# Performance work log

Measured on AMD Instinct MI355X. Metric: run time of the kernel, lower is better.

## Reference

```python
import jax, jax.numpy as jnp
import numpy as np

B, T, V, S, I, G = 2, 4096, 1024, 256, 2048, 128


def setup_inputs() -> dict:
    key = jax.random.key(0)
    ks = jax.random.split(key, 10)
    n = lambda k, shape, std: jax.random.normal(k, shape, dtype=jnp.float32) * std
    return {
        "x": jax.random.normal(ks[0], (B, T, V), dtype=jnp.float32),
        # shared CausalMemory projections (torch Linear weight layout [out,in])
        "Wq": n(ks[1], (S, V), 0.02),
        "Wk": n(ks[2], (S, V), 0.02),
        "Wv": n(ks[3], (S, V), 0.02),
        "Wo": n(ks[4], (V, S), 0.02),
        # Delta
        "delta_logits": jnp.full((V,), 4.0, dtype=jnp.float32),
        "delta_scale": jnp.float32(0.1),
        # Theta / Gamma decay params
        "theta_decay": jnp.float32(4.0),
        "theta_scale": jnp.float32(0.1),
        "gamma_decay": jnp.float32(1.0),
        "gamma_scale": jnp.float32(0.1),
        # Alpha gate
        "alpha_down": n(ks[5], (G, V), 0.02),
        "alpha_up": n(ks[6], (V, G), 0.01),
        "alpha_up_b": jnp.full((V,), 2.0, dtype=jnp.float32),
        # Beta MLP
        "beta_down": n(ks[7], (I, V), 0.02),
        "beta_up": n(ks[8], (V, I), 0.02),
        "beta_bias": jnp.zeros((I,), dtype=jnp.float32),
        "beta_scale": jnp.float32(0.1),
    }


def _rmsnorm(x):
    eps = jnp.finfo(x.dtype).eps
    return x * jax.lax.rsqrt(jnp.mean(x * x, axis=-1, keepdims=True) + eps)


def _delta(x, decay_logits, scale):
    # causal EMA via weighted cumsum, matching torch reference exactly
    t = x.shape[1]
    decay = jax.nn.sigmoid(decay_logits)
    log_decay = jnp.log(jnp.clip(decay, 1e-06))
    steps = jnp.arange(t, dtype=x.dtype)[::-1]            # [T]
    w = jnp.exp(steps[:, None] * log_decay[None, :])      # [T,V]
    cum = jnp.cumsum(x * w[None], axis=1)
    cum = jnp.concatenate([jnp.zeros_like(cum[:, :1]), cum[:, :-1]], axis=1)
    return cum / jnp.clip(w[None], 1e-08) * scale


def _memory(x, Wq, Wk, Wv, Wo, decay_logit, scale):
    t = x.shape[1]
    q = x @ Wq.T
    k = x @ Wk.T
    v = x @ Wv.T
    scores = jnp.einsum("btd,bsd->bts", q, k)             # [B,T,T]
    decay = jax.nn.sigmoid(decay_logit)
    pos = jnp.arange(t)
    diff = pos[None, :] - pos[:, None]                    # j - i
    w = decay ** jnp.clip(diff.astype(x.dtype) - 1.0, 0.0, None) * (diff > 0)
    retrieved = jnp.einsum("bts,bsd->btd", scores * w[None], v)
    return (retrieved @ Wo.T) * scale


def _alpha(x, down, up, up_b):
    gate = jax.nn.sigmoid((x @ down.T) @ up.T + up_b)
    return x * gate


def _beta(x, down, up, bias, scale):
    h = jax.nn.gelu(x @ down.T + bias, approximate=False)
    return (h @ up.T) * scale


def reference(x, Wq, Wk, Wv, Wo, delta_logits, delta_scale, theta_decay,
              theta_scale, gamma_decay, gamma_scale, alpha_down, alpha_up,
              alpha_up_b, beta_down, beta_up, beta_bias, beta_scale):
    x = x + _delta(_rmsnorm(x), delta_logits, delta_scale)
    x = x + _memory(_rmsnorm(x), Wq, Wk, Wv, Wo, theta_decay, theta_scale)
    x = _alpha(x, alpha_down, alpha_up, alpha_up_b)
    x = x + _beta(_rmsnorm(x), beta_down, beta_up, beta_bias, beta_scale)
    x = x + _memory(_rmsnorm(x), Wq, Wk, Wv, Wo, gamma_decay, gamma_scale)
    return x
```

## Files before the change

kernel.cpp:

```cpp
#include <hip/hip_runtime.h>

typedef __attribute__((ext_vector_type(8))) short s16x8;
typedef __attribute__((ext_vector_type(4))) float f32x4;
typedef unsigned short u16;

#define DEV __device__ __forceinline__

DEV u16 f2b(float f) {
  unsigned u = __builtin_bit_cast(unsigned, f);
  unsigned r = (u + 0x7FFFu + ((u >> 16) & 1u)) >> 16;
  return (u16)r;
}
DEV float b2f(u16 h) { return __builtin_bit_cast(float, (unsigned)h << 16); }
DEV f32x4 mfma16(s16x8 a, s16x8 b, f32x4 c) {
  return __builtin_amdgcn_mfma_f32_16x16x32_bf16(a, b, c, 0, 0, 0);
}
DEV float sigmoidf_(float x) { return 1.0f / (1.0f + expf(-x)); }

DEV void g2l16(const u16* g, u16* l) {
  __builtin_amdgcn_global_load_lds((const __attribute__((address_space(1))) void*)g,
                                   (__attribute__((address_space(3))) void*)l, 16, 0, 0);
}

#define BAR() __builtin_amdgcn_s_barrier()
#define WAITV8() asm volatile("s_waitcnt vmcnt(8)" ::: "memory")
#define WAITV4() asm volatile("s_waitcnt vmcnt(4)" ::: "memory")
#define WAITV0() asm volatile("s_waitcnt vmcnt(0)" ::: "memory")
#define WAITL0()                                         \
  do {                                                   \
    asm volatile("s_waitcnt lgkmcnt(0)" ::: "memory");   \
    __builtin_amdgcn_sched_barrier(0);                   \
  } while (0)

__global__ __launch_bounds__(256) void cast_all(
    const float* __restrict__ Wq, const float* __restrict__ Wk, const float* __restrict__ Wv,
    const float* __restrict__ Wo, const float* __restrict__ adw, const float* __restrict__ auw,
    const float* __restrict__ bdw, const float* __restrict__ buw,
    u16* __restrict__ Wqkvb, u16* __restrict__ Wob, u16* __restrict__ adb,
    u16* __restrict__ aub, u16* __restrict__ bdb, u16* __restrict__ bub) {
  const int b = blockIdx.x;
  const float* s;
  u16* d;
  int rb;
  if (b < 768) {
    s = (b < 256) ? Wq : (b < 512) ? Wk : Wv;
    rb = (b < 256) ? b : (b < 512) ? (b - 256) : (b - 512);
    d = Wqkvb + ((b < 256) ? 0 : (b < 512) ? 262144 : 524288);
  } else if (b < 1024) { s = Wo;  d = Wob; rb = b - 768; }
  else if (b < 1152)   { s = adw; d = adb; rb = b - 1024; }
  else if (b < 1280)   { s = auw; d = aub; rb = b - 1152; }
  else if (b < 3328)   { s = bdw; d = bdb; rb = b - 1280; }
  else                 { s = buw; d = bub; rb = b - 3328; }
  size_t i = ((size_t)rb * 256 + threadIdx.x) * 4;
  float4 v = *(const float4*)(s + i);
  ushort4 p; p.x = f2b(v.x); p.y = f2b(v.y); p.z = f2b(v.z); p.w = f2b(v.w);
  *(ushort4*)(d + i) = p;
}

__global__ __launch_bounds__(256) void rmsnorm_k(const float* __restrict__ x, u16* __restrict__ y) {
  const size_t row = blockIdx.x;
  const int tid = threadIdx.x;
  float4 v = ((const float4*)(x + row * 1024))[tid];
  float ss = v.x * v.x + v.y * v.y + v.z * v.z + v.w * v.w;
#pragma unroll
  for (int o = 32; o >= 1; o >>= 1) ss += __shfl_xor(ss, o);
  __shared__ float red[4];
  if ((tid & 63) == 0) red[tid >> 6] = ss;
  __syncthreads();
  float tot = red[0] + red[1] + red[2] + red[3];
  float rn = rsqrtf(tot * (1.0f / 1024.0f) + 1.1920929e-7f);
  ushort4 p;
  p.x = f2b(v.x * rn); p.y = f2b(v.y * rn); p.z = f2b(v.z * rn); p.w = f2b(v.w * rn);
  *(ushort4*)(y + row * 1024 + tid * 4) = p;
}

__global__ __launch_bounds__(256)
void delta_partial(const u16* __restrict__ y, const float* __restrict__ logits, float* __restrict__ Pp) {
  const int v = blockIdx.x * 256 + threadIdx.x;
  const int c = blockIdx.y, b = blockIdx.z;
  const float dec = sigmoidf_(logits[v]);
  const float ldc = logf(fmaxf(dec, 1e-6f));
  const float dc = expf(ldc);
  const u16* yp = y + ((size_t)b * 4096 + c * 128) * 1024 + v;
  float wv = expf((float)(4095 - (c * 128 + 127)) * ldc);
  float acc = 0.0f;
  for (int t = 127; t >= 0; --t) {
    acc += b2f(yp[(size_t)t * 1024]) * wv;
    wv *= dc;
  }
  Pp[((size_t)b * 32 + c) * 1024 + v] = acc;
}

__global__ __launch_bounds__(256) void delta_scan(float* __restrict__ Pp) {
  const int v = blockIdx.x * 256 + threadIdx.x;
  const int b = blockIdx.y;
  float run = 0.0f;
  for (int c = 0; c < 32; ++c) {
    size_t i = ((size_t)b * 32 + c) * 1024 + v;
    float t = Pp[i];
    Pp[i] = run;
    run += t;
  }
}

__global__ __launch_bounds__(256)
void delta_apply(const float* __restrict__ x0, const u16* __restrict__ y,
                 const float* __restrict__ logits, const float* __restrict__ scale_p,
                 const float* __restrict__ Pp, float* __restrict__ x1) {
  const int v = blockIdx.x * 256 + threadIdx.x;
  const int c = blockIdx.y, b = blockIdx.z;
  const float dec = sigmoidf_(logits[v]);
  const float ldc = logf(fmaxf(dec, 1e-6f));
  const float dc = expf(ldc);
  const float invd = expf(-ldc);
  const float sc = scale_p[0];
  float wv = expf((float)(4095 - c * 128) * ldc);
  float iw = expf(-(float)(4095 - c * 128) * ldc);
  float carry = Pp[((size_t)b * 32 + c) * 1024 + v];
  size_t base = ((size_t)b * 4096 + c * 128) * 1024 + v;
  for (int t = 0; t < 128; ++t) {
    size_t idx = base + (size_t)t * 1024;
    x1[idx] = x0[idx] + carry * fminf(iw, 1e8f) * sc;
    carry += b2f(y[idx]) * wv;
    wv *= invd;
    iw *= dc;
  }
}

template <int EPI>
__global__ __launch_bounds__(256, 2)
void pgemm(const u16* __restrict__ A, const u16* __restrict__ Bw,
           int M, int N, int K,
           u16* __restrict__ Cb,
           const float* __restrict__ Xin, float* __restrict__ Xout,
           u16* __restrict__ Xb16,
           const float* __restrict__ bias, const float* __restrict__ scale_p,
           u16* __restrict__ P1, u16* __restrict__ P2, u16* __restrict__ P3) {
  __shared__ u16 sm[32768];
  const int tid = threadIdx.x;
  const int wid = tid >> 6, lane = tid & 63;
  const int gx = gridDim.x;
  const int id = blockIdx.y * gx + blockIdx.x;
  const int q8 = (gx * gridDim.y) >> 3;
  const int nid = (id & 7) * q8 + (id >> 3);
  const int bx = nid % gx, by = nid / gx;
  const int n0 = bx * 128, m0 = by * 128;
  const int wm = (wid >> 1) * 64, wn = (wid & 1) * 64;
  const int lr = lane & 15, lkc = lane >> 4;
  const int sw = lr & 7;
  const int c0 = (lkc ^ sw) * 8, c1 = ((lkc + 4) ^ sw) * 8;
  const int NT = K >> 6;
  const int srow = lane >> 3;
  const int scol = ((lane & 7) ^ srow) * 8;
  const u16* Ag = A + (size_t)(m0 + wid * 8 + srow) * K + scol;
  const u16* Bg = Bw + (size_t)(n0 + wid * 8 + srow) * K + scol;
  u16* const AL0 = sm;          u16* const BL0 = sm + 8192;
  u16* const AL1 = sm + 16384;  u16* const BL1 = sm + 24576;

  f32x4 acc[4][4] = {};

  auto STA = [&](int tau) {
    const u16* g = Ag + (size_t)tau * 64;
    u16* l = ((tau & 1) ? AL1 : AL0) + wid * 512;
#pragma unroll
    for (int c = 0; c < 4; ++c) g2l16(g + (size_t)c * 32 * K, l + c * 2048);
  };
  auto STB = [&](int tau) {
    const u16* g = Bg + (size_t)tau * 64;
    u16* l = ((tau & 1) ? BL1 : BL0) + wid * 512;
#pragma unroll
    for (int c = 0; c < 4; ++c) g2l16(g + (size_t)c * 32 * K, l + c * 2048);
  };
  auto RDA = [&](int tau, s16x8 (&d)[4][2]) {
    const u16* Ab = (tau & 1) ? AL1 : AL0;
#pragma unroll
    for (int i = 0; i < 4; ++i) {
      int base = (wm + i * 16 + lr) * 64;
      d[i][0] = *(const s16x8*)&Ab[base + c0];
      d[i][1] = *(const s16x8*)&Ab[base + c1];
    }
  };
  auto RDB = [&](int tau, int h, s16x8 (&d)[2][2]) {
    const u16* Bb = (tau & 1) ? BL1 : BL0;
#pragma unroll
    for (int j = 0; j < 2; ++j) {
      int base = (wn + h * 32 + j * 16 + lr) * 64;
      d[j][0] = *(const s16x8*)&Bb[base + c0];
      d[j][1] = *(const s16x8*)&Bb[base + c1];
    }
  };
  auto MM = [&](s16x8 (&Ar)[4][2], s16x8 (&Br)[2][2], int jo) {
    __builtin_amdgcn_s_setprio(1);
#pragma unroll
    for (int i = 0; i < 4; ++i)
#pragma unroll
      for (int j = 0; j < 2; ++j) {
        acc[i][jo + j] = mfma16(Ar[i][0], Br[j][0], acc[i][jo + j]);
        acc[i][jo + j] = mfma16(Ar[i][1], Br[j][1], acc[i][jo + j]);
      }
    __builtin_amdgcn_s_setprio(0);
  };

  s16x8 Ae[4][2], Ao[4][2], B0r[2][2], B1r[2][2];
  STA(0); STB(0);
  if (NT > 1) { STA(1); STB(1); }
  WAITV8(); BAR();
  RDA(0, Ae); RDB(0, 0, B0r);

  for (int t = 0; t < NT; t += 2) {
    RDB(t, 1, B1r);
    if (t + 2 < NT) STA(t + 2);
    BAR(); WAITL0();
    MM(Ae, B0r, 0);
    BAR();
    if (t + 2 < NT) { STB(t + 2); WAITV8(); } else { WAITV0(); }
    BAR();
    if (t + 1 < NT) { RDA(t + 1, Ao); RDB(t + 1, 0, B0r); }
    WAITL0();
    MM(Ae, B1r, 2);
    BAR();
    if (t + 1 >= NT) break;
    RDB(t + 1, 1, B1r);
    if (t + 3 < NT) STA(t + 3);
    BAR(); WAITL0();
    MM(Ao, B0r, 0);
    BAR();
    if (t + 3 < NT) { STB(t + 3); WAITV8(); } else { WAITV0(); }
    BAR();
    if (t + 2 < NT) { RDA(t + 2, Ae); RDB(t + 2, 0, B0r); }
    WAITL0();
    MM(Ao, B1r, 2);
    BAR();
  }

  float* tl = (float*)(void*)sm + wid * 1088;

  if constexpr (EPI == 5) {
    if (bx < 4) {
      u16* dst = (bx < 2) ? Cb : P1;
      const int nb = (bx & 1) * 128;
#pragma unroll
      for (int i = 0; i < 4; ++i) {
#pragma unroll
        for (int j = 0; j < 4; ++j)
#pragma unroll
          for (int r = 0; r < 4; ++r)
            tl[(lkc * 4 + r) * 68 + j * 16 + lr] = acc[i][j][r];
#pragma unroll
        for (int p = 0; p < 4; ++p) {
          const int row = p * 4 + lkc, nl = lr * 4;
          f32x4 v = *(const f32x4*)&tl[row * 68 + nl];
          const int m = m0 + wm + i * 16 + row;
          ushort4 o = {f2b(v[0]), f2b(v[1]), f2b(v[2]), f2b(v[3])};
          *(ushort4*)&dst[(size_t)m * 256 + nb + wn + nl] = o;
        }
      }
      if (bx >= 2) {
        const float ld5 = logf(sigmoidf_(scale_p[0]));
        u16* CT = sm;
        __syncthreads();
#pragma unroll
        for (int i = 0; i < 4; ++i)
#pragma unroll
          for (int j = 0; j < 4; ++j)
#pragma unroll
            for (int r = 0; r < 4; ++r) {
              int ml = wm + i * 16 + lkc * 4 + r;
              int nl = wn + j * 16 + lr;
              float g = expf(ld5 * (float)(ml & 63));
              CT[nl * 136 + ml] = f2b(acc[i][j][r] * g);
            }
        __syncthreads();
        int d = tid >> 1, off = (tid & 1) * 64;
        size_t base = ((size_t)(m0 >> 12) * 256 + (bx - 2) * 128 + d) * 4096 + (m0 & 4095) + off;
#pragma unroll
        for (int p = 0; p < 8; ++p)
          *(uint4*)&P3[base + p * 8] = *(const uint4*)&CT[d * 136 + off + p * 8];
      }
    } else {
      u16* CT = sm;
      __syncthreads();
#pragma unroll
      for (int i = 0; i < 4; ++i)
#pragma unroll
        for (int j = 0; j < 4; ++j)
#pragma unroll
          for (int r = 0; r < 4; ++r) {
            int ml = wm + i * 16 + lkc * 4 + r;
            int nl = wn + j * 16 + lr;
            CT[nl * 136 + ml] = f2b(acc[i][j][r]);
          }
      __syncthreads();
      int d = tid >> 1, off = (tid & 1) * 64;
      size_t base = ((size_t)(m0 >> 12) * 256 + (bx - 4) * 128 + d) * 4096 + (m0 & 4095) + off;
#pragma unroll
      for (int p = 0; p < 8; ++p)
        *(uint4*)&P2[base + p * 8] = *(const uint4*)&CT[d * 136 + off + p * 8];
    }
  } else {
    const float sc = (EPI == 2) ? scale_p[0] : 0.0f;
    float4 xpf[16];
    float4 bpf = {0.0f, 0.0f, 0.0f, 0.0f};
    if constexpr (EPI == 2 || EPI == 4) {
#pragma unroll
      for (int i = 0; i < 4; ++i)
#pragma unroll
        for (int p = 0; p < 4; ++p) {
          const int m = m0 + wm + i * 16 + p * 4 + lkc;
          xpf[i * 4 + p] = *(const float4*)&Xin[(size_t)m * N + n0 + wn + lr * 4];
        }
    }
    if constexpr (EPI == 3 || EPI == 4) bpf = *(const float4*)&bias[n0 + wn + lr * 4];
#pragma unroll
    for (int i = 0; i < 4; ++i) {
#pragma unroll
      for (int j = 0; j < 4; ++j)
#pragma unroll
        for (int r = 0; r < 4; ++r)
          tl[(lkc * 4 + r) * 68 + j * 16 + lr] = acc[i][j][r];
#pragma unroll
      for (int p = 0; p < 4; ++p) {
        const int row = p * 4 + lkc, nl = lr * 4;
        f32x4 v = *(const f32x4*)&tl[row * 68 + nl];
        const int m = m0 + wm + i * 16 + row;
        const int n = n0 + wn + nl;
        const size_t idx = (size_t)m * N + n;
        if constexpr (EPI == 0) {
          ushort4 o = {f2b(v[0]), f2b(v[1]), f2b(v[2]), f2b(v[3])};
          *(ushort4*)&Cb[idx] = o;
        } else if constexpr (EPI == 2) {
          float4 x = xpf[i * 4 + p];
          float4 o = {x.x + v[0] * sc, x.y + v[1] * sc, x.z + v[2] * sc, x.w + v[3] * sc};
          *(float4*)&Xout[idx] = o;
          if (Xb16) {
            ushort4 ob = {f2b(o.x), f2b(o.y), f2b(o.z), f2b(o.w)};
            *(ushort4*)&Xb16[idx] = ob;
          }
        } else if constexpr (EPI == 3) {
          float g0 = v[0] + bpf.x, g1 = v[1] + bpf.y, g2 = v[2] + bpf.z, g3 = v[3] + bpf.w;
          ushort4 o;
          o.x = f2b(g0 * sigmoidf_(1.59576912f * fmaf(0.044715f * g0, g0 * g0, g0)));
          o.y = f2b(g1 * sigmoidf_(1.59576912f * fmaf(0.044715f * g1, g1 * g1, g1)));
          o.z = f2b(g2 * sigmoidf_(1.59576912f * fmaf(0.044715f * g2, g2 * g2, g2)));
          o.w = f2b(g3 * sigmoidf_(1.59576912f * fmaf(0.044715f * g3, g3 * g3, g3)));
          *(ushort4*)&Cb[idx] = o;
        } else {
          float4 x = xpf[i * 4 + p];
          float4 o = {x.x * sigmoidf_(v[0] + bpf.x), x.y * sigmoidf_(v[1] + bpf.y),
                      x.z * sigmoidf_(v[2] + bpf.z), x.w * sigmoidf_(v[3] + bpf.w)};
          *(float4*)&Xout[idx] = o;
        }
      }
    }
  }
}

__global__ __launch_bounds__(256, 2)
void chunk_G(const u16* __restrict__ vT, const u16* __restrict__ kTs, float* __restrict__ Gp) {
  __shared__ u16 sm2[16384];
  const int c = blockIdx.x, eh = blockIdx.y >> 1, dh = blockIdx.y & 1, b = blockIdx.z;
  const int tid = threadIdx.x, wid = tid >> 6, lane = tid & 63;
  u16* AL = sm2; u16* BL = sm2 + 8192;
  const u16* As = vT + (size_t)(b * 256 + eh * 128) * 4096 + c * 64;
  const u16* Bs = kTs + (size_t)(b * 256 + dh * 128) * 4096 + c * 64;
  const int r8 = lane >> 3, sc8 = ((lane & 7) ^ (lane >> 3)) * 8;
#pragma unroll
  for (int p = 0; p < 4; ++p) {
    int ch = p * 4 + wid;
    int row = ch * 8 + r8;
    g2l16(As + (size_t)row * 4096 + sc8, AL + ch * 512);
    g2l16(Bs + (size_t)row * 4096 + sc8, BL + ch * 512);
  }
  __syncthreads();
  const int wm = (wid >> 1) * 64, wn = (wid & 1) * 64;
  const int lr = lane & 15, lkc = lane >> 4, sw = lr & 7;
  const int c0 = (lkc ^ sw) * 8, c1 = ((lkc + 4) ^ sw) * 8;
  s16x8 af[4][2], bf[4][2];
#pragma unroll
  for (int i = 0; i < 4; ++i) {
    int ba = (wm + i * 16 + lr) * 64;
    af[i][0] = *(const s16x8*)&AL[ba + c0];
    af[i][1] = *(const s16x8*)&AL[ba + c1];
    int bb = (wn + i * 16 + lr) * 64;
    bf[i][0] = *(const s16x8*)&BL[bb + c0];
    bf[i][1] = *(const s16x8*)&BL[bb + c1];
  }
  f32x4 acc[4][4] = {};
#pragma unroll
  for (int i = 0; i < 4; ++i)
#pragma unroll
    for (int j = 0; j < 4; ++j) {
      acc[i][j] = mfma16(af[i][0], bf[j][0], acc[i][j]);
      acc[i][j] = mfma16(af[i][1], bf[j][1], acc[i][j]);
    }
  float* Gb = Gp + (size_t)(b * 64 + c) * 65536;
#pragma unroll
  for (int i = 0; i < 4; ++i)
#pragma unroll
    for (int j = 0; j < 4; ++j)
#pragma unroll
      for (int r = 0; r < 4; ++r) {
        int e = eh * 128 + wm + i * 16 + lkc * 4 + r;
        int d = dh * 128 + wn + j * 16 + lr;
        Gb[(size_t)e * 256 + d] = acc[i][j][r];
      }
}

__global__ __launch_bounds__(256)
void scan_M(const float* __restrict__ Gp, u16* __restrict__ Mb, const float* __restrict__ dlogit) {
  const int b = blockIdx.y;
  const size_t idx = (size_t)blockIdx.x * 256 + threadIdx.x;
  const float ld = logf(sigmoidf_(dlogit[0]));
  const float g64 = expf(64.0f * ld);
  const float* G = Gp + (size_t)b * 64 * 65536 + idx;
  u16* M = Mb + (size_t)b * 64 * 65536 + idx;
  float m = 0.0f;
  M[(size_t)63 * 65536] = 0;
  float g = G[(size_t)63 * 65536];
  for (int c = 62; c >= 0; --c) {
    float gn = 0.0f;
    if (c > 0) gn = G[(size_t)c * 65536];
    m = g + g64 * m;
    M[(size_t)c * 65536] = f2b(m);
    g = gn;
  }
}

__global__ __launch_bounds__(256, 2)
void chunk_R(const u16* __restrict__ q, const u16* __restrict__ k,
             const u16* __restrict__ vT, const u16* __restrict__ Mb,
             u16* __restrict__ R, const float* __restrict__ dlogit) {
  __shared__ u16 qL[16384];
  __shared__ u16 shA[16384];
  const int c = blockIdx.x, eh = blockIdx.y, b = blockIdx.z;
  const int tid = threadIdx.x, wid = tid >> 6, lane = tid & 63;
  const float ld = logf(sigmoidf_(dlogit[0]));
  const int r8 = lane >> 3, sc8 = ((lane & 7) ^ (lane >> 3)) * 8;
  const int lr = lane & 15, lkc = lane >> 4, g4 = lkc * 4;
  const int sw = lr & 7;
  const int c0 = (lkc ^ sw) * 8, c1 = ((lkc + 4) ^ sw) * 8;

  const u16* qsrc = q + ((size_t)b * 4096 + c * 64) * 256;
  const u16* ksrc = k + ((size_t)b * 4096 + c * 64) * 256;
  const u16* msrc = Mb + ((size_t)(b * 64 + c) * 256 + eh * 128) * 256;
  const u16* vsrc = vT + (size_t)(b * 256 + eh * 128) * 4096 + c * 64;

#pragma unroll
  for (int kt = 0; kt < 4; ++kt)
#pragma unroll
    for (int p = 0; p < 2; ++p) {
      int ch = p * 4 + wid;
      int row = ch * 8 + r8;
      g2l16(qsrc + (size_t)row * 256 + kt * 64 + sc8, qL + kt * 4096 + ch * 512);
    }
#pragma unroll
  for (int p = 0; p < 4; ++p) {
    int ch = p * 4 + wid;
    int row = ch * 8 + r8;
    g2l16(msrc + (size_t)row * 256 + sc8, shA + ch * 512);
  }
  f32x4 accx[4][2] = {};
  for (int dt = 0; dt < 4; ++dt) {
    if (dt < 3) {
      u16* dst = shA + ((dt + 1) & 1) * 8192;
#pragma unroll
      for (int p = 0; p < 4; ++p) {
        int ch = p * 4 + wid;
        int row = ch * 8 + r8;
        g2l16(msrc + (size_t)row * 256 + (dt + 1) * 64 + sc8, dst + ch * 512);
      }
      WAITV4();
    } else {
      WAITV0();
    }
    BAR();
    const u16* mt = shA + (dt & 1) * 8192;
    const u16* qt = qL + dt * 4096;
    s16x8 aq[4][2], bm[2][2];
#pragma unroll
    for (int i = 0; i < 4; ++i) {
      int ba = (i * 16 + lr) * 64;
      aq[i][0] = *(const s16x8*)&qt[ba + c0];
      aq[i][1] = *(const s16x8*)&qt[ba + c1];
    }
#pragma unroll
    for (int j = 0; j < 2; ++j) {
      int ba = (wid * 32 + j * 16 + lr) * 64;
      bm[j][0] = *(const s16x8*)&mt[ba + c0];
      bm[j][1] = *(const s16x8*)&mt[ba + c1];
    }
#pragma unroll
    for (int i = 0; i < 4; ++i)
#pragma unroll
      for (int j = 0; j < 2; ++j) {
        accx[i][j] = mfma16(aq[i][0], bm[j][0], accx[i][j]);
        accx[i][j] = mfma16(aq[i][1], bm[j][1], accx[i][j]);
      }
    BAR();
  }
#pragma unroll
  for (int kt = 0; kt < 4; ++kt)
#pragma unroll
    for (int p = 0; p < 2; ++p) {
      int ch = p * 4 + wid;
      int row = ch * 8 + r8;
      g2l16(ksrc + (size_t)row * 256 + kt * 64 + sc8, shA + kt * 4096 + ch * 512);
    }
  __syncthreads();
  f32x4 accs[4] = {};
#pragma unroll
  for (int kt = 0; kt < 4; ++kt) {
    const u16* qt = qL + kt * 4096;
    const u16* klt = shA + kt * 4096;
    s16x8 aq[4][2], bk[2];
#pragma unroll
    for (int i = 0; i < 4; ++i) {
      int ba = (i * 16 + lr) * 64;
      aq[i][0] = *(const s16x8*)&qt[ba + c0];
      aq[i][1] = *(const s16x8*)&qt[ba + c1];
    }
    {
      int ba = (wid * 16 + lr) * 64;
      bk[0] = *(const s16x8*)&klt[ba + c0];
      bk[1] = *(const s16x8*)&klt[ba + c1];
    }
#pragma unroll
    for (int i = 0; i < 4; ++i) {
      accs[i] = mfma16(aq[i][0], bk[0], accs[i]);
      accs[i] = mfma16(aq[i][1], bk[1], accs[i]);
    }
  }
  __syncthreads();
  u16* PL = shA;
  u16* vTL = shA + 4608;
#pragma unroll
  for (int p = 0; p < 4; ++p) {
    int ch = p * 4 + wid;
    int row = ch * 8 + r8;
    g2l16(vsrc + (size_t)row * 4096 + sc8, vTL + ch * 512);
  }
#pragma unroll
  for (int i = 0; i < 4; ++i)
#pragma unroll
    for (int r = 0; r < 4; ++r) {
      int gi = i * 16 + g4 + r;
      int gj = wid * 16 + lr;
      float pw = (gj > gi) ? expf(ld * (float)(gj - gi - 1)) : 0.0f;
      PL[gi * 72 + gj] = f2b(accs[i][r] * pw);
    }
  __syncthreads();
  f32x4 acci[4][2] = {};
  {
    s16x8 pa[4][2], bv[2][2];
#pragma unroll
    for (int i = 0; i < 4; ++i) {
      pa[i][0] = *(const s16x8*)&PL[(i * 16 + lr) * 72 + lkc * 8];
      pa[i][1] = *(const s16x8*)&PL[(i * 16 + lr) * 72 + 32 + lkc * 8];
    }
#pragma unroll
    for (int j = 0; j < 2; ++j) {
      int ba = (wid * 32 + j * 16 + lr) * 64;
      bv[j][0] = *(const s16x8*)&vTL[ba + c0];
      bv[j][1] = *(const s16x8*)&vTL[ba + c1];
    }
#pragma unroll
    for (int i = 0; i < 4; ++i)
#pragma unroll
      for (int j = 0; j < 2; ++j) {
        acci[i][j] = mfma16(pa[i][0], bv[j][0], acci[i][j]);
        acci[i][j] = mfma16(pa[i][1], bv[j][1], acci[i][j]);
      }
  }
  u16* Ro = R + ((size_t)b * 4096 + c * 64) * 256 + eh * 128;
#pragma unroll
  for (int i = 0; i < 4; ++i)
#pragma unroll
    for (int r = 0; r < 4; ++r) {
      int gi = i * 16 + g4 + r;
      float xf = expf(ld * (float)(63 - gi));
#pragma unroll
      for (int j = 0; j < 2; ++j) {
        int ge = wid * 32 + j * 16 + lr;
        Ro[(size_t)gi * 256 + ge] = f2b(acci[i][j][r] + xf * accx[i][j][r]);
      }
    }
}

extern "C" void kernel_launch(void* const* d_in, const int* in_sizes, int n_in,
                              void* d_out, int out_size, void* d_ws, size_t ws_size,
                              hipStream_t stream) {
  const float* x0 = (const float*)d_in[0];
  const float* Wq = (const float*)d_in[1];
  const float* Wk = (const float*)d_in[2];
  const float* Wv = (const float*)d_in[3];
  const float* Wo = (const float*)d_in[4];
  const float* dlog = (const float*)d_in[5];
  const float* dscale = (const float*)d_in[6];
  const float* th_dec = (const float*)d_in[7];
  const float* th_sc = (const float*)d_in[8];
  const float* ga_dec = (const float*)d_in[9];
  const float* ga_sc = (const float*)d_in[10];
  const float* adw = (const float*)d_in[11];
  const float* auw = (const float*)d_in[12];
  const float* a_upb = (const float*)d_in[13];
  const float* bdw = (const float*)d_in[14];
  const float* buw = (const float*)d_in[15];
  const float* bbias = (const float*)d_in[16];
  const float* bscale = (const float*)d_in[17];

  char* w = (char*)d_ws;
  float* xA = (float*)w;
  u16* y = (u16*)(w + 33554432);
  u16* xb = (u16*)(w + 50331648);
  u16* qb = (u16*)(w + 67108864);
  u16* kb = (u16*)(w + 71303168);
  u16* vT = (u16*)(w + 75497472);
  u16* Rb = (u16*)(w + 79691776);
  u16* gb = (u16*)(w + 83886080);
  u16* hb = (u16*)(w + 85983232);
  float* Gp = (float*)hb;
  u16* Mbuf = y;
  u16* kTs = xb;
  float* Pp = (float*)(w + 119537664);
  u16* Wqkvb = (u16*)(w + 119799808);
  u16* Wob = (u16*)(w + 121372672);
  u16* adb = (u16*)(w + 121896960);
  u16* aub = (u16*)(w + 122159104);
  u16* bdb = (u16*)(w + 122421248);
  u16* bub = (u16*)(w + 126615552);
  float* xB = (float*)d_out;

  cast_all<<<5376, 256, 0, stream>>>(Wq, Wk, Wv, Wo, adw, auw, bdw, buw,
                                     Wqkvb, Wob, adb, aub, bdb, bub);

  rmsnorm_k<<<8192, 256, 0, stream>>>(x0, y);
  delta_partial<<<dim3(4, 32, 2), 256, 0, stream>>>(y, dlog, Pp);
  delta_scan<<<dim3(4, 2), 256, 0, stream>>>(Pp);
  delta_apply<<<dim3(4, 32, 2), 256, 0, stream>>>(x0, y, dlog, dscale, Pp, xA);

  rmsnorm_k<<<8192, 256, 0, stream>>>(xA, y);
  pgemm<5><<<dim3(6, 64), 256, 0, stream>>>(y, Wqkvb, 8192, 768, 1024, qb, nullptr, nullptr, nullptr, nullptr, th_dec, kb, vT, kTs);
  chunk_G<<<dim3(64, 4, 2), 256, 0, stream>>>(vT, kTs, Gp);
  scan_M<<<dim3(256, 2), 256, 0, stream>>>(Gp, Mbuf, th_dec);
  chunk_R<<<dim3(64, 2, 2), 256, 0, stream>>>(qb, kb, vT, Mbuf, Rb, th_dec);
  pgemm<2><<<dim3(8, 64), 256, 0, stream>>>(Rb, Wob, 8192, 1024, 256, nullptr, xA, xB, xb, nullptr, th_sc, nullptr, nullptr, nullptr);

  pgemm<0><<<dim3(1, 64), 256, 0, stream>>>(xb, adb, 8192, 128, 1024, gb, nullptr, nullptr, nullptr, nullptr, nullptr, nullptr, nullptr, nullptr);
  pgemm<4><<<dim3(8, 64), 256, 0, stream>>>(gb, aub, 8192, 1024, 128, nullptr, xB, xA, nullptr, a_upb, nullptr, nullptr, nullptr, nullptr);

  rmsnorm_k<<<8192, 256, 0, stream>>>(xA, y);
  pgemm<3><<<dim3(16, 64), 256, 0, stream>>>(y, bdb, 8192, 2048, 1024, hb, nullptr, nullptr, nullptr, bbias, nullptr, nullptr, nullptr, nullptr);
  pgemm<2><<<dim3(8, 64), 256, 0, stream>>>(hb, bub, 8192, 1024, 2048, nullptr, xA, xB, nullptr, nullptr, bscale, nullptr, nullptr, nullptr);

  rmsnorm_k<<<8192, 256, 0, stream>>>(xB, y);
  pgemm<5><<<dim3(6, 64), 256, 0, stream>>>(y, Wqkvb, 8192, 768, 1024, qb, nullptr, nullptr, nullptr, nullptr, ga_dec, kb, vT, kTs);
  chunk_G<<<dim3(64, 4, 2), 256, 0, stream>>>(vT, kTs, Gp);
  scan_M<<<dim3(256, 2), 256, 0, stream>>>(Gp, Mbuf, ga_dec);
  chunk_R<<<dim3(64, 2, 2), 256, 0, stream>>>(qb, kb, vT, Mbuf, Rb, ga_dec);
  pgemm<2><<<dim3(8, 64), 256, 0, stream>>>(Rb, Wob, 8192, 1024, 256, nullptr, xB, xB, nullptr, nullptr, ga_sc, nullptr, nullptr, nullptr);
}
```

Baseline: 326.4 us.

## Replace double-buffered pgemm pipeline with single-buffer loop at higher occupancy

```diff
diff --git a/kernel.cpp b/kernel.cpp
--- a/kernel.cpp
+++ b/kernel.cpp
@@ -22,15 +22,9 @@
                                    (__attribute__((address_space(3))) void*)l, 16, 0, 0);
 }
 
-#define BAR() __builtin_amdgcn_s_barrier()
-#define WAITV8() asm volatile("s_waitcnt vmcnt(8)" ::: "memory")
 #define WAITV4() asm volatile("s_waitcnt vmcnt(4)" ::: "memory")
 #define WAITV0() asm volatile("s_waitcnt vmcnt(0)" ::: "memory")
-#define WAITL0()                                         \
-  do {                                                   \
-    asm volatile("s_waitcnt lgkmcnt(0)" ::: "memory");   \
-    __builtin_amdgcn_sched_barrier(0);                   \
-  } while (0)
+#define BAR() __builtin_amdgcn_s_barrier()
 
 __global__ __launch_bounds__(256) void cast_all(
     const float* __restrict__ Wq, const float* __restrict__ Wk, const float* __restrict__ Wv,
@@ -128,7 +122,7 @@
 }
 
 template <int EPI>
-__global__ __launch_bounds__(256, 2)
+__global__ __launch_bounds__(256, 4)
 void pgemm(const u16* __restrict__ A, const u16* __restrict__ Bw,
            int M, int N, int K,
            u16* __restrict__ Cb,
@@ -136,7 +130,7 @@
            u16* __restrict__ Xb16,
            const float* __restrict__ bias, const float* __restrict__ scale_p,
            u16* __restrict__ P1, u16* __restrict__ P2, u16* __restrict__ P3) {
-  __shared__ u16 sm[32768];
+  __shared__ u16 sm[17472];
   const int tid = threadIdx.x;
   const int wid = tid >> 6, lane = tid & 63;
   const int gx = gridDim.x;
@@ -154,83 +148,49 @@
   const int scol = ((lane & 7) ^ srow) * 8;
   const u16* Ag = A + (size_t)(m0 + wid * 8 + srow) * K + scol;
   const u16* Bg = Bw + (size_t)(n0 + wid * 8 + srow) * K + scol;
-  u16* const AL0 = sm;          u16* const BL0 = sm + 8192;
-  u16* const AL1 = sm + 16384;  u16* const BL1 = sm + 24576;
+  u16* const As = sm;
+  u16* const Bs = sm + 8192;
 
   f32x4 acc[4][4] = {};
 
-  auto STA = [&](int tau) {
-    const u16* g = Ag + (size_t)tau * 64;
-    u16* l = ((tau & 1) ? AL1 : AL0) + wid * 512;
-#pragma unroll
-    for (int c = 0; c < 4; ++c) g2l16(g + (size_t)c * 32 * K, l + c * 2048);
-  };
-  auto STB = [&](int tau) {
-    const u16* g = Bg + (size_t)tau * 64;
-    u16* l = ((tau & 1) ? BL1 : BL0) + wid * 512;
-#pragma unroll
-    for (int c = 0; c < 4; ++c) g2l16(g + (size_t)c * 32 * K, l + c * 2048);
-  };
-  auto RDA = [&](int tau, s16x8 (&d)[4][2]) {
-    const u16* Ab = (tau & 1) ? AL1 : AL0;
+  for (int t = 0; t < NT; ++t) {
+    {
+      const u16* ga = Ag + (size_t)t * 64;
+      const u16* gb = Bg + (size_t)t * 64;
+      u16* la = As + wid * 512;
+      u16* lb = Bs + wid * 512;
+#pragma unroll
+      for (int c = 0; c < 4; ++c) {
+        g2l16(ga + (size_t)c * 32 * K, la + c * 2048);
+        g2l16(gb + (size_t)c * 32 * K, lb + c * 2048);
+      }
+    }
+    __syncthreads();
+    s16x8 af[4][2], bfr[2][2][2];
 #pragma unroll
     for (int i = 0; i < 4; ++i) {
       int base = (wm + i * 16 + lr) * 64;
-      d[i][0] = *(const s16x8*)&Ab[base + c0];
-      d[i][1] = *(const s16x8*)&Ab[base + c1];
-    }
-  };
-  auto RDB = [&](int tau, int h, s16x8 (&d)[2][2]) {
-    const u16* Bb = (tau & 1) ? BL1 : BL0;
-#pragma unroll
-    for (int j = 0; j < 2; ++j) {
-      int base = (wn + h * 32 + j * 16 + lr) * 64;
-      d[j][0] = *(const s16x8*)&Bb[base + c0];
-      d[j][1] = *(const s16x8*)&Bb[base + c1];
-    }
-  };
-  auto MM = [&](s16x8 (&Ar)[4][2], s16x8 (&Br)[2][2], int jo) {
-    __builtin_amdgcn_s_setprio(1);
+      af[i][0] = *(const s16x8*)&As[base + c0];
+      af[i][1] = *(const s16x8*)&As[base + c1];
+    }
+#pragma unroll
+    for (int h = 0; h < 2; ++h)
+#pragma unroll
+      for (int j = 0; j < 2; ++j) {
+        int base = (wn + h * 32 + j * 16 + lr) * 64;
+        bfr[h][j][0] = *(const s16x8*)&Bs[base + c0];
+        bfr[h][j][1] = *(const s16x8*)&Bs[base + c1];
+      }
 #pragma unroll
     for (int i = 0; i < 4; ++i)
 #pragma unroll
-      for (int j = 0; j < 2; ++j) {
-        acc[i][jo + j] = mfma16(Ar[i][0], Br[j][0], acc[i][jo + j]);
-        acc[i][jo + j] = mfma16(Ar[i][1], Br[j][1], acc[i][jo + j]);
-      }
-    __builtin_amdgcn_s_setprio(0);
-  };
-
-  s16x8 Ae[4][2], Ao[4][2], B0r[2][2], B1r[2][2];
-  STA(0); STB(0);
-  if (NT > 1) { STA(1); STB(1); }
-  WAITV8(); BAR();
-  RDA(0, Ae); RDB(0, 0, B0r);
-
-  for (int t = 0; t < NT; t += 2) {
-    RDB(t, 1, B1r);
-    if (t + 2 < NT) STA(t + 2);
-    BAR(); WAITL0();
-    MM(Ae, B0r, 0);
-    BAR();
-    if (t + 2 < NT) { STB(t + 2); WAITV8(); } else { WAITV0(); }
-    BAR();
-    if (t + 1 < NT) { RDA(t + 1, Ao); RDB(t + 1, 0, B0r); }
-    WAITL0();
-    MM(Ae, B1r, 2);
-    BAR();
-    if (t + 1 >= NT) break;
-    RDB(t + 1, 1, B1r);
-    if (t + 3 < NT) STA(t + 3);
-    BAR(); WAITL0();
-    MM(Ao, B0r, 0);
-    BAR();
-    if (t + 3 < NT) { STB(t + 3); WAITV8(); } else { WAITV0(); }
-    BAR();
-    if (t + 2 < NT) { RDA(t + 2, Ae); RDB(t + 2, 0, B0r); }
-    WAITL0();
-    MM(Ao, B1r, 2);
-    BAR();
+      for (int h = 0; h < 2; ++h)
+#pragma unroll
+        for (int j = 0; j < 2; ++j) {
+          acc[i][h * 2 + j] = mfma16(af[i][0], bfr[h][j][0], acc[i][h * 2 + j]);
+          acc[i][h * 2 + j] = mfma16(af[i][1], bfr[h][j][1], acc[i][h * 2 + j]);
+        }
+    __syncthreads();
   }
 
   float* tl = (float*)(void*)sm + wid * 1088;
@@ -299,17 +259,7 @@
     }
   } else {
     const float sc = (EPI == 2) ? scale_p[0] : 0.0f;
-    float4 xpf[16];
     float4 bpf = {0.0f, 0.0f, 0.0f, 0.0f};
-    if constexpr (EPI == 2 || EPI == 4) {
-#pragma unroll
-      for (int i = 0; i < 4; ++i)
-#pragma unroll
-        for (int p = 0; p < 4; ++p) {
-          const int m = m0 + wm + i * 16 + p * 4 + lkc;
-          xpf[i * 4 + p] = *(const float4*)&Xin[(size_t)m * N + n0 + wn + lr * 4];
-        }
-    }
     if constexpr (EPI == 3 || EPI == 4) bpf = *(const float4*)&bias[n0 + wn + lr * 4];
 #pragma unroll
     for (int i = 0; i < 4; ++i) {
@@ -329,7 +279,7 @@
           ushort4 o = {f2b(v[0]), f2b(v[1]), f2b(v[2]), f2b(v[3])};
           *(ushort4*)&Cb[idx] = o;
         } else if constexpr (EPI == 2) {
-          float4 x = xpf[i * 4 + p];
+          float4 x = *(const float4*)&Xin[idx];
           float4 o = {x.x + v[0] * sc, x.y + v[1] * sc, x.z + v[2] * sc, x.w + v[3] * sc};
           *(float4*)&Xout[idx] = o;
           if (Xb16) {
@@ -345,7 +295,7 @@
           o.w = f2b(g3 * sigmoidf_(1.59576912f * fmaf(0.044715f * g3, g3 * g3, g3)));
           *(ushort4*)&Cb[idx] = o;
         } else {
-          float4 x = xpf[i * 4 + p];
+          float4 x = *(const float4*)&Xin[idx];
           float4 o = {x.x * sigmoidf_(v[0] + bpf.x), x.y * sigmoidf_(v[1] + bpf.y),
                       x.z * sigmoidf_(v[2] + bpf.z), x.w * sigmoidf_(v[3] + bpf.w)};
           *(float4*)&Xout[idx] = o;
```

Result: slower. 342.5 us (+4.9%).

## Add single-buffered high-occupancy GEMM variant and route long-K GEMMs to it

Applied to the files above, without the earlier changes.

```diff
diff --git a/kernel.cpp b/kernel.cpp
--- a/kernel.cpp
+++ b/kernel.cpp
@@ -128,14 +128,197 @@
 }
 
 template <int EPI>
+__global__ __launch_bounds__(256, 4)
+void pgemm_s(const u16* __restrict__ A, const u16* __restrict__ Bw,
+             int M, int N, int K,
+             u16* __restrict__ Cb,
+             const float* __restrict__ Xin, float* __restrict__ Xout,
+             u16* __restrict__ Xb16,
+             const float* __restrict__ bias, const float* __restrict__ scale_p,
+             u16* __restrict__ P1, u16* __restrict__ P2, u16* __restrict__ P3) {
+  __shared__ u16 sm[17472];
+  const int tid = threadIdx.x;
+  const int wid = tid >> 6, lane = tid & 63;
+  const int gx = gridDim.x;
+  const int id = blockIdx.y * gx + blockIdx.x;
+  const int q8 = (gx * gridDim.y) >> 3;
+  const int nid = (id & 7) * q8 + (id >> 3);
+  const int bx = nid % gx, by = nid / gx;
+  const int n0 = bx * 128, m0 = by * 128;
+  const int wm = (wid >> 1) * 64, wn = (wid & 1) * 64;
+  const int lr = lane & 15, lkc = lane >> 4;
+  const int sw = lr & 7;
+  const int c0 = (lkc ^ sw) * 8, c1 = ((lkc + 4) ^ sw) * 8;
+  const int NT = K >> 6;
+  const int srow = lane >> 3;
+  const int scol = ((lane & 7) ^ srow) * 8;
+  const u16* Ag = A + (size_t)(m0 + wid * 8 + srow) * K + scol;
+  const u16* Bg = Bw + (size_t)(n0 + wid * 8 + srow) * K + scol;
+  u16* const As = sm;
+  u16* const Bs = sm + 8192;
+
+  f32x4 acc[4][4] = {};
+
+  for (int t = 0; t < NT; ++t) {
+    {
+      const u16* ga = Ag + (size_t)t * 64;
+      const u16* gb = Bg + (size_t)t * 64;
+      u16* la = As + wid * 512;
+      u16* lb = Bs + wid * 512;
+#pragma unroll
+      for (int c = 0; c < 4; ++c) {
+        g2l16(ga + (size_t)c * 32 * K, la + c * 2048);
+        g2l16(gb + (size_t)c * 32 * K, lb + c * 2048);
+      }
+    }
+    __syncthreads();
+    s16x8 af[4][2], bfr[2][2][2];
+#pragma unroll
+    for (int i = 0; i < 4; ++i) {
+      int base = (wm + i * 16 + lr) * 64;
+      af[i][0] = *(const s16x8*)&As[base + c0];
+      af[i][1] = *(const s16x8*)&As[base + c1];
+    }
+#pragma unroll
+    for (int h = 0; h < 2; ++h)
+#pragma unroll
+      for (int j = 0; j < 2; ++j) {
+        int base = (wn + h * 32 + j * 16 + lr) * 64;
+        bfr[h][j][0] = *(const s16x8*)&Bs[base + c0];
+        bfr[h][j][1] = *(const s16x8*)&Bs[base + c1];
+      }
+#pragma unroll
+    for (int i = 0; i < 4; ++i)
+#pragma unroll
+      for (int h = 0; h < 2; ++h)
+#pragma unroll
+        for (int j = 0; j < 2; ++j) {
+          acc[i][h * 2 + j] = mfma16(af[i][0], bfr[h][j][0], acc[i][h * 2 + j]);
+          acc[i][h * 2 + j] = mfma16(af[i][1], bfr[h][j][1], acc[i][h * 2 + j]);
+        }
+    __syncthreads();
+  }
+
+  float* tl = (float*)(void*)sm + wid * 1088;
+
+  if constexpr (EPI == 5) {
+    if (bx < 4) {
+      u16* dst = (bx < 2) ? Cb : P1;
+      const int nb = (bx & 1) * 128;
+#pragma unroll
+      for (int i = 0; i < 4; ++i) {
+#pragma unroll
+        for (int j = 0; j < 4; ++j)
+#pragma unroll
+          for (int r = 0; r < 4; ++r)
+            tl[(lkc * 4 + r) * 68 + j * 16 + lr] = acc[i][j][r];
+#pragma unroll
+        for (int p = 0; p < 4; ++p) {
+          const int row = p * 4 + lkc, nl = lr * 4;
+          f32x4 v = *(const f32x4*)&tl[row * 68 + nl];
+          const int m = m0 + wm + i * 16 + row;
+          ushort4 o = {f2b(v[0]), f2b(v[1]), f2b(v[2]), f2b(v[3])};
+          *(ushort4*)&dst[(size_t)m * 256 + nb + wn + nl] = o;
+        }
+      }
+      if (bx >= 2) {
+        const float ld5 = logf(sigmoidf_(scale_p[0]));
+        u16* CT = sm;
+        __syncthreads();
+#pragma unroll
+        for (int i = 0; i < 4; ++i)
+#pragma unroll
+          for (int j = 0; j < 4; ++j)
+#pragma unroll
+            for (int r = 0; r < 4; ++r) {
+              int ml = wm + i * 16 + lkc * 4 + r;
+              int nl = wn + j * 16 + lr;
+              float g = expf(ld5 * (float)(ml & 63));
+              CT[nl * 136 + ml] = f2b(acc[i][j][r] * g);
+            }
+        __syncthreads();
+        int d = tid >> 1, off = (tid & 1) * 64;
+        size_t base = ((size_t)(m0 >> 12) * 256 + (bx - 2) * 128 + d) * 4096 + (m0 & 4095) + off;
+#pragma unroll
+        for (int p = 0; p < 8; ++p)
+          *(uint4*)&P3[base + p * 8] = *(const uint4*)&CT[d * 136 + off + p * 8];
+      }
+    } else {
+      u16* CT = sm;
+      __syncthreads();
+#pragma unroll
+      for (int i = 0; i < 4; ++i)
+#pragma unroll
+        for (int j = 0; j < 4; ++j)
+#pragma unroll
+          for (int r = 0; r < 4; ++r) {
+            int ml = wm + i * 16 + lkc * 4 + r;
+            int nl = wn + j * 16 + lr;
+            CT[nl * 136 + ml] = f2b(acc[i][j][r]);
+          }
+      __syncthreads();
+      int d = tid >> 1, off = (tid & 1) * 64;
+      size_t base = ((size_t)(m0 >> 12) * 256 + (bx - 4) * 128 + d) * 4096 + (m0 & 4095) + off;
+#pragma unroll
+      for (int p = 0; p < 8; ++p)
+        *(uint4*)&P2[base + p * 8] = *(const uint4*)&CT[d * 136 + off + p * 8];
+    }
+  } else {
+    const float sc = (EPI == 2) ? scale_p[0] : 0.0f;
+    float4 bpf = {0.0f, 0.0f, 0.0f, 0.0f};
+    if constexpr (EPI == 3 || EPI == 4) bpf = *(const float4*)&bias[n0 + wn + lr * 4];
+#pragma unroll
+    for (int i = 0; i < 4; ++i) {
+#pragma unroll
+      for (int j = 0; j < 4; ++j)
+#pragma unroll
+        for (int r = 0; r < 4; ++r)
+          tl[(lkc * 4 + r) * 68 + j * 16 + lr] = acc[i][j][r];
+#pragma unroll
+      for (int p = 0; p < 4; ++p) {
+        const int row = p * 4 + lkc, nl = lr * 4;
+        f32x4 v = *(const f32x4*)&tl[row * 68 + nl];
+        const int m = m0 + wm + i * 16 + row;
+        const int n = n0 + wn + nl;
+        const size_t idx = (size_t)m * N + n;
+        if constexpr (EPI == 0) {
+          ushort4 o = {f2b(v[0]), f2b(v[1]), f2b(v[2]), f2b(v[3])};
+          *(ushort4*)&Cb[idx] = o;
+        } else if constexpr (EPI == 2) {
+          float4 x = *(const float4*)&Xin[idx];
+          float4 o = {x.x + v[0] * sc, x.y + v[1] * sc, x.z + v[2] * sc, x.w + v[3] * sc};
+          *(float4*)&Xout[idx] = o;
+          if (Xb16) {
+            ushort4 ob = {f2b(o.x), f2b(o.y), f2b(o.z), f2b(o.w)};
+            *(ushort4*)&Xb16[idx] = ob;
+          }
+        } else if constexpr (EPI == 3) {
+          float g0 = v[0] + bpf.x, g1 = v[1] + bpf.y, g2 = v[2] + bpf.z, g3 = v[3] + bpf.w;
+          ushort4 o;
+          o.x = f2b(g0 * sigmoidf_(1.59576912f * fmaf(0.044715f * g0, g0 * g0, g0)));
+          o.y = f2b(g1 * sigmoidf_(1.59576912f * fmaf(0.044715f * g1, g1 * g1, g1)));
+          o.z = f2b(g2 * sigmoidf_(1.59576912f * fmaf(0.044715f * g2, g2 * g2, g2)));
+          o.w = f2b(g3 * sigmoidf_(1.59576912f * fmaf(0.044715f * g3, g3 * g3, g3)));
+          *(ushort4*)&Cb[idx] = o;
+        } else {
+          float4 x = *(const float4*)&Xin[idx];
+          float4 o = {x.x * sigmoidf_(v[0] + bpf.x), x.y * sigmoidf_(v[1] + bpf.y),
+                      x.z * sigmoidf_(v[2] + bpf.z), x.w * sigmoidf_(v[3] + bpf.w)};
+          *(float4*)&Xout[idx] = o;
+        }
+      }
+    }
+  }
+}
+
+template <int EPI>
 __global__ __launch_bounds__(256, 2)
-void pgemm(const u16* __restrict__ A, const u16* __restrict__ Bw,
-           int M, int N, int K,
-           u16* __restrict__ Cb,
-           const float* __restrict__ Xin, float* __restrict__ Xout,
-           u16* __restrict__ Xb16,
-           const float* __restrict__ bias, const float* __restrict__ scale_p,
-           u16* __restrict__ P1, u16* __restrict__ P2, u16* __restrict__ P3) {
+void pgemm_d(const u16* __restrict__ A, const u16* __restrict__ Bw,
+             int M, int N, int K,
+             u16* __restrict__ Cb,
+             const float* __restrict__ Xin, float* __restrict__ Xout,
+             u16* __restrict__ Xb16,
+             const float* __restrict__ bias, const float* __restrict__ scale_p) {
   __shared__ u16 sm[32768];
   const int tid = threadIdx.x;
   const int wid = tid >> 6, lane = tid & 63;
@@ -234,122 +417,47 @@
   }
 
   float* tl = (float*)(void*)sm + wid * 1088;
-
-  if constexpr (EPI == 5) {
-    if (bx < 4) {
-      u16* dst = (bx < 2) ? Cb : P1;
-      const int nb = (bx & 1) * 128;
-#pragma unroll
-      for (int i = 0; i < 4; ++i) {
-#pragma unroll
-        for (int j = 0; j < 4; ++j)
-#pragma unroll
-          for (int r = 0; r < 4; ++r)
-            tl[(lkc * 4 + r) * 68 + j * 16 + lr] = acc[i][j][r];
-#pragma unroll
-        for (int p = 0; p < 4; ++p) {
-          const int row = p * 4 + lkc, nl = lr * 4;
-          f32x4 v = *(const f32x4*)&tl[row * 68 + nl];
-          const int m = m0 + wm + i * 16 + row;
-          ushort4 o = {f2b(v[0]), f2b(v[1]), f2b(v[2]), f2b(v[3])};
-          *(ushort4*)&dst[(size_t)m * 256 + nb + wn + nl] = o;
+  const float sc = (EPI == 2) ? scale_p[0] : 0.0f;
+  float4 bpf = {0.0f, 0.0f, 0.0f, 0.0f};
+  if constexpr (EPI == 3 || EPI == 4) bpf = *(const float4*)&bias[n0 + wn + lr * 4];
+#pragma unroll
+  for (int i = 0; i < 4; ++i) {
+#pragma unroll
+    for (int j = 0; j < 4; ++j)
+#pragma unroll
+      for (int r = 0; r < 4; ++r)
+        tl[(lkc * 4 + r) * 68 + j * 16 + lr] = acc[i][j][r];
+#pragma unroll
+    for (int p = 0; p < 4; ++p) {
+      const int row = p * 4 + lkc, nl = lr * 4;
+      f32x4 v = *(const f32x4*)&tl[row * 68 + nl];
+      const int m = m0 + wm + i * 16 + row;
+      const int n = n0 + wn + nl;
+      const size_t idx = (size_t)m * N + n;
+      if constexpr (EPI == 0) {
+        ushort4 o = {f2b(v[0]), f2b(v[1]), f2b(v[2]), f2b(v[3])};
+        *(ushort4*)&Cb[idx] = o;
+      } else if constexpr (EPI == 2) {
+        float4 x = *(const float4*)&Xin[idx];
+        float4 o = {x.x + v[0] * sc, x.y + v[1] * sc, x.z + v[2] * sc, x.w + v[3] * sc};
+        *(float4*)&Xout[idx] = o;
+        if (Xb16) {
+          ushort4 ob = {f2b(o.x), f2b(o.y), f2b(o.z), f2b(o.w)};
+          *(ushort4*)&Xb16[idx] = ob;
         }
-      }
-      if (bx >= 2) {
-        const float ld5 = logf(sigmoidf_(scale_p[0]));
-        u16* CT = sm;
-        __syncthreads();
-#pragma unroll
-        for (int i = 0; i < 4; ++i)
-#pragma unroll
-          for (int j = 0; j < 4; ++j)
-#pragma unroll
-            for (int r = 0; r < 4; ++r) {
-              int ml = wm + i * 16 + lkc * 4 + r;
-              int nl = wn + j * 16 + lr;
-              float g = expf(ld5 * (float)(ml & 63));
-              CT[nl * 136 + ml] = f2b(acc[i][j][r] * g);
-            }
-        __syncthreads();
-        int d = tid >> 1, off = (tid & 1) * 64;
-        size_t base = ((size_t)(m0 >> 12) * 256 + (bx - 2) * 128 + d) * 4096 + (m0 & 4095) + off;
-#pragma unroll
-        for (int p = 0; p < 8; ++p)
-          *(uint4*)&P3[base + p * 8] = *(const uint4*)&CT[d * 136 + off + p * 8];
-      }
-    } else {
-      u16* CT = sm;
-      __syncthreads();
-#pragma unroll
-      for (int i = 0; i < 4; ++i)
-#pragma unroll
-        for (int j = 0; j < 4; ++j)
-#pragma unroll
-          for (int r = 0; r < 4; ++r) {
-            int ml = wm + i * 16 + lkc * 4 + r;
-            int nl = wn + j * 16 + lr;
-            CT[nl * 136 + ml] = f2b(acc[i][j][r]);
-          }
-      __syncthreads();
-      int d = tid >> 1, off = (tid & 1) * 64;
-      size_t base = ((size_t)(m0 >> 12) * 256 + (bx - 4) * 128 + d) * 4096 + (m0 & 4095) + off;
-#pragma unroll
-      for (int p = 0; p < 8; ++p)
-        *(uint4*)&P2[base + p * 8] = *(const uint4*)&CT[d * 136 + off + p * 8];
-    }
-  } else {
-    const float sc = (EPI == 2) ? scale_p[0] : 0.0f;
-    float4 xpf[16];
-    float4 bpf = {0.0f, 0.0f, 0.0f, 0.0f};
-    if constexpr (EPI == 2 || EPI == 4) {
-#pragma unroll
-      for (int i = 0; i < 4; ++i)
-#pragma unroll
-        for (int p = 0; p < 4; ++p) {
-          const int m = m0 + wm + i * 16 + p * 4 + lkc;
-          xpf[i * 4 + p] = *(const float4*)&Xin[(size_t)m * N + n0 + wn + lr * 4];
-        }
-    }
-    if constexpr (EPI == 3 || EPI == 4) bpf = *(const float4*)&bias[n0 + wn + lr * 4];
-#pragma unroll
-    for (int i = 0; i < 4; ++i) {
-#pragma unroll
-      for (int j = 0; j < 4; ++j)
-#pragma unroll
-        for (int r = 0; r < 4; ++r)
-          tl[(lkc * 4 + r) * 68 + j * 16 + lr] = acc[i][j][r];
-#pragma unroll
-      for (int p = 0; p < 4; ++p) {
-        const int row = p * 4 + lkc, nl = lr * 4;
-        f32x4 v = *(const f32x4*)&tl[row * 68 + nl];
-        const int m = m0 + wm + i * 16 + row;
-        const int n = n0 + wn + nl;
-        const size_t idx = (size_t)m * N + n;
-        if constexpr (EPI == 0) {
-          ushort4 o = {f2b(v[0]), f2b(v[1]), f2b(v[2]), f2b(v[3])};
-          *(ushort4*)&Cb[idx] = o;
-        } else if constexpr (EPI == 2) {
-          float4 x = xpf[i * 4 + p];
-          float4 o = {x.x + v[0] * sc, x.y + v[1] * sc, x.z + v[2] * sc, x.w + v[3] * sc};
-          *(float4*)&Xout[idx] = o;
-          if (Xb16) {
-            ushort4 ob = {f2b(o.x), f2b(o.y), f2b(o.z), f2b(o.w)};
-            *(ushort4*)&Xb16[idx] = ob;
-          }
-        } else if constexpr (EPI == 3) {
-          float g0 = v[0] + bpf.x, g1 = v[1] + bpf.y, g2 = v[2] + bpf.z, g3 = v[3] + bpf.w;
-          ushort4 o;
-          o.x = f2b(g0 * sigmoidf_(1.59576912f * fmaf(0.044715f * g0, g0 * g0, g0)));
-          o.y = f2b(g1 * sigmoidf_(1.59576912f * fmaf(0.044715f * g1, g1 * g1, g1)));
-          o.z = f2b(g2 * sigmoidf_(1.59576912f * fmaf(0.044715f * g2, g2 * g2, g2)));
-          o.w = f2b(g3 * sigmoidf_(1.59576912f * fmaf(0.044715f * g3, g3 * g3, g3)));
-          *(ushort4*)&Cb[idx] = o;
-        } else {
-          float4 x = xpf[i * 4 + p];
-          float4 o = {x.x * sigmoidf_(v[0] + bpf.x), x.y * sigmoidf_(v[1] + bpf.y),
-                      x.z * sigmoidf_(v[2] + bpf.z), x.w * sigmoidf_(v[3] + bpf.w)};
-          *(float4*)&Xout[idx] = o;
-        }
+      } else if constexpr (EPI == 3) {
+        float g0 = v[0] + bpf.x, g1 = v[1] + bpf.y, g2 = v[2] + bpf.z, g3 = v[3] + bpf.w;
+        ushort4 o;
+        o.x = f2b(g0 * sigmoidf_(1.59576912f * fmaf(0.044715f * g0, g0 * g0, g0)));
+        o.y = f2b(g1 * sigmoidf_(1.59576912f * fmaf(0.044715f * g1, g1 * g1, g1)));
+        o.z = f2b(g2 * sigmoidf_(1.59576912f * fmaf(0.044715f * g2, g2 * g2, g2)));
+        o.w = f2b(g3 * sigmoidf_(1.59576912f * fmaf(0.044715f * g3, g3 * g3, g3)));
+        *(ushort4*)&Cb[idx] = o;
+      } else {
+        float4 x = *(const float4*)&Xin[idx];
+        float4 o = {x.x * sigmoidf_(v[0] + bpf.x), x.y * sigmoidf_(v[1] + bpf.y),
+                    x.z * sigmoidf_(v[2] + bpf.z), x.w * sigmoidf_(v[3] + bpf.w)};
+        *(float4*)&Xout[idx] = o;
       }
     }
   }
@@ -639,23 +747,23 @@
   delta_apply<<<dim3(4, 32, 2), 256, 0, stream>>>(x0, y, dlog, dscale, Pp, xA);
 
   rmsnorm_k<<<8192, 256, 0, stream>>>(xA, y);
-  pgemm<5><<<dim3(6, 64), 256, 0, stream>>>(y, Wqkvb, 8192, 768, 1024, qb, nullptr, nullptr, nullptr, nullptr, th_dec, kb, vT, kTs);
+  pgemm_s<5><<<dim3(6, 64), 256, 0, stream>>>(y, Wqkvb, 8192, 768, 1024, qb, nullptr, nullptr, nullptr, nullptr, th_dec, kb, vT, kTs);
   chunk_G<<<dim3(64, 4, 2), 256, 0, stream>>>(vT, kTs, Gp);
   scan_M<<<dim3(256, 2), 256, 0, stream>>>(Gp, Mbuf, th_dec);
   chunk_R<<<dim3(64, 2, 2), 256, 0, stream>>>(qb, kb, vT, Mbuf, Rb, th_dec);
-  pgemm<2><<<dim3(8, 64), 256, 0, stream>>>(Rb, Wob, 8192, 1024, 256, nullptr, xA, xB, xb, nullptr, th_sc, nullptr, nullptr, nullptr);
-
-  pgemm<0><<<dim3(1, 64), 256, 0, stream>>>(xb, adb, 8192, 128, 1024, gb, nullptr, nullptr, nullptr, nullptr, nullptr, nullptr, nullptr, nullptr);
-  pgemm<4><<<dim3(8, 64), 256, 0, stream>>>(gb, aub, 8192, 1024, 128, nullptr, xB, xA, nullptr, a_upb, nullptr, nullptr, nullptr, nullptr);
+  pgemm_d<2><<<dim3(8, 64), 256, 0, stream>>>(Rb, Wob, 8192, 1024, 256, nullptr, xA, xB, xb, nullptr, th_sc);
+
+  pgemm_s<0><<<dim3(1, 64), 256, 0, stream>>>(xb, adb, 8192, 128, 1024, gb, nullptr, nullptr, nullptr, nullptr, nullptr, nullptr, nullptr, nullptr);
+  pgemm_d<4><<<dim3(8, 64), 256, 0, stream>>>(gb, aub, 8192, 1024, 128, nullptr, xB, xA, nullptr, a_upb, nullptr);
 
   rmsnorm_k<<<8192, 256, 0, stream>>>(xA, y);
-  pgemm<3><<<dim3(16, 64), 256, 0, stream>>>(y, bdb, 8192, 2048, 1024, hb, nullptr, nullptr, nullptr, bbias, nullptr, nullptr, nullptr, nullptr);
-  pgemm<2><<<dim3(8, 64), 256, 0, stream>>>(hb, bub, 8192, 1024, 2048, nullptr, xA, xB, nullptr, nullptr, bscale, nullptr, nullptr, nullptr);
+  pgemm_s<3><<<dim3(16, 64), 256, 0, stream>>>(y, bdb, 8192, 2048, 1024, hb, nullptr, nullptr, nullptr, bbias, nullptr, nullptr, nullptr, nullptr);
+  pgemm_s<2><<<dim3(8, 64), 256, 0, stream>>>(hb, bub, 8192, 1024, 2048, nullptr, xA, xB, nullptr, nullptr, bscale, nullptr, nullptr, nullptr);
 
   rmsnorm_k<<<8192, 256, 0, stream>>>(xB, y);
-  pgemm<5><<<dim3(6, 64), 256, 0, stream>>>(y, Wqkvb, 8192, 768, 1024, qb, nullptr, nullptr, nullptr, nullptr, ga_dec, kb, vT, kTs);
+  pgemm_s<5><<<dim3(6, 64), 256, 0, stream>>>(y, Wqkvb, 8192, 768, 1024, qb, nullptr, nullptr, nullptr, nullptr, ga_dec, kb, vT, kTs);
   chunk_G<<<dim3(64, 4, 2), 256, 0, stream>>>(vT, kTs, Gp);
   scan_M<<<dim3(256, 2), 256, 0, stream>>>(Gp, Mbuf, ga_dec);
   chunk_R<<<dim3(64, 2, 2), 256, 0, stream>>>(qb, kb, vT, Mbuf, Rb, ga_dec);
-  pgemm<2><<<dim3(8, 64), 256, 0, stream>>>(Rb, Wob, 8192, 1024, 256, nullptr, xB, xB, nullptr, nullptr, ga_sc, nullptr, nullptr, nullptr);
-}
+  pgemm_d<2><<<dim3(8, 64), 256, 0, stream>>>(Rb, Wob, 8192, 1024, 256, nullptr, xB, xB, nullptr, nullptr, ga_sc);
+}
```

Result: slower. 342.7 us (+5.0%).
